# Performance work log

Hardware: AMD Instinct MI355X
Metric: run time of the kernel (lower is better)

The kernel has to match this reference:

```python
import jax, jax.numpy as jnp
import numpy as np

HEADS, DH, M_LAND, PINV_ITERS, LN_EPS = 8, 64, 256, 6, 1e-5


def layer_norm(x, g, b):
    mu = x.mean(-1, keepdims=True)
    var = ((x - mu) ** 2).mean(-1, keepdims=True)
    return (x - mu) * jax.lax.rsqrt(var + LN_EPS) * g + b


def moore_penrose_pinv(x, iters=PINV_ITERS):
    # x: (h, m, m). Iterative Newton-Schulz style pinv (lucidrains).
    abs_x = jnp.abs(x)
    col = abs_x.sum(-1)
    row = abs_x.sum(-2)
    z = jnp.swapaxes(x, -1, -2) / (jnp.max(col) * jnp.max(row))
    I = jnp.eye(x.shape[-1], dtype=x.dtype)
    for _ in range(iters):
        xz = x @ z
        z = 0.25 * z @ (13.0 * I - xz @ (15.0 * I - xz @ (7.0 * I - xz)))
    return z


def nystrom_attention(x, qkv_w, out_w, out_b, res_w):
    # x: (n, dim). No mask, eval mode (dropout off).
    n, dim = x.shape
    pad = (-n) % M_LAND
    xp = jnp.pad(x, ((pad, 0), (0, 0)))  # pad at sequence START, as in original
    n_p = n + pad
    l = n_p // M_LAND  # tokens per landmark
    qkv = xp @ qkv_w  # (n_p, 3*h*dh)
    q, k, v = jnp.split(qkv, 3, axis=-1)
    split = lambda t: t.reshape(n_p, HEADS, DH).transpose(1, 0, 2)  # (h, n_p, dh)
    q, k, v = split(q), split(k), split(v)
    q = q * (DH ** -0.5)
    q_l = q.reshape(HEADS, M_LAND, l, DH).mean(axis=2)  # (h, m, dh)
    k_l = k.reshape(HEADS, M_LAND, l, DH).mean(axis=2)
    sim1 = jnp.einsum('hid,hjd->hij', q, k_l)    # (h, n_p, m)
    sim2 = jnp.einsum('hid,hjd->hij', q_l, k_l)  # (h, m, m)
    sim3 = jnp.einsum('hid,hjd->hij', q_l, k)    # (h, m, n_p)
    a1 = jax.nn.softmax(sim1, axis=-1)
    a2 = jax.nn.softmax(sim2, axis=-1)
    a3 = jax.nn.softmax(sim3, axis=-1)
    a2_inv = moore_penrose_pinv(a2)
    out = a1 @ (a2_inv @ (a3 @ v))  # (h, n_p, dh)
    # residual depthwise conv over sequence dim, kernel 33, per head
    res = jax.lax.conv_general_dilated(
        v[None], res_w, (1, 1), ((16, 16), (0, 0)),
        feature_group_count=HEADS, dimension_numbers=('NCHW', 'OIHW', 'NCHW'))[0]
    out = out + res
    out = out.transpose(1, 0, 2).reshape(n_p, HEADS * DH)
    out = out @ out_w + out_b
    return out[-n:]  # drop the leading pad


def ppeg(x, w7, b7, w5, b5, w3, b3, H, W):
    cls_tok, feat = x[0], x[1:]
    C = feat.shape[1]
    img = feat.T.reshape(1, C, H, W)
    def dw(w, b, p):
        y = jax.lax.conv_general_dilated(
            img, w, (1, 1), ((p, p), (p, p)),
            feature_group_count=C, dimension_numbers=('NCHW', 'OIHW', 'NCHW'))
        return y + b.reshape(1, C, 1, 1)
    out = img + dw(w7, b7, 3) + dw(w5, b5, 2) + dw(w3, b3, 1)
    out = out[0].reshape(C, H * W).T
    return jnp.concatenate([cls_tok[None], out], axis=0)


def forward(h, fc1_w, fc1_b, cls_token, l1_ln_g, l1_ln_b, l1_qkv_w, l1_out_w, l1_out_b, l1_res_w,
            conv7_w, conv7_b, conv5_w, conv5_b, conv3_w, conv3_b,
            l2_ln_g, l2_ln_b, l2_qkv_w, l2_out_w, l2_out_b, l2_res_w,
            norm_g, norm_b, fc2_w, fc2_b):
    x = jax.nn.relu(h @ fc1_w + fc1_b)  # (N, 512)
    N = x.shape[0]
    Hs = Ws = int(np.ceil(np.sqrt(N)))  # N chosen perfect square -> add_length == 0
    x = jnp.concatenate([cls_token, x], axis=0)  # (N+1, 512)
    x = x + nystrom_attention(layer_norm(x, l1_ln_g, l1_ln_b), l1_qkv_w, l1_out_w, l1_out_b, l1_res_w)
    x = ppeg(x, conv7_w, conv7_b, conv5_w, conv5_b, conv3_w, conv3_b, Hs, Ws)
    x = x + nystrom_attention(layer_norm(x, l2_ln_g, l2_ln_b), l2_qkv_w, l2_out_w, l2_out_b, l2_res_w)
    x = layer_norm(x, norm_g, norm_b)[0]  # cls token readout
    return x @ fc2_w + fc2_b  # (n_classes,)


def setup_inputs() -> dict:
    key = jax.random.key(0)
    ks = jax.random.split(key, 16)
    nrm = lambda k, s, sc=0.02: jax.random.normal(k, s, jnp.float32) * sc
    D = 512
    return {
        'h': jax.random.normal(ks[0], (16384, 2048), jnp.float32),
        'fc1_w': nrm(ks[1], (2048, D)), 'fc1_b': jnp.zeros((D,), jnp.float32),
        'cls_token': nrm(ks[2], (1, D), 1.0),
        'l1_ln_g': jnp.ones((D,), jnp.float32), 'l1_ln_b': jnp.zeros((D,), jnp.float32),
        'l1_qkv_w': nrm(ks[3], (D, 3 * D)),
        'l1_out_w': nrm(ks[4], (D, D)), 'l1_out_b': jnp.zeros((D,), jnp.float32),
        'l1_res_w': nrm(ks[5], (HEADS, 1, 33, 1), 0.05),
        'conv7_w': nrm(ks[6], (D, 1, 7, 7), 0.05), 'conv7_b': jnp.zeros((D,), jnp.float32),
        'conv5_w': nrm(ks[7], (D, 1, 5, 5), 0.05), 'conv5_b': jnp.zeros((D,), jnp.float32),
        'conv3_w': nrm(ks[8], (D, 1, 3, 3), 0.05), 'conv3_b': jnp.zeros((D,), jnp.float32),
        'l2_ln_g': jnp.ones((D,), jnp.float32), 'l2_ln_b': jnp.zeros((D,), jnp.float32),
        'l2_qkv_w': nrm(ks[9], (D, 3 * D)),
        'l2_out_w': nrm(ks[10], (D, D)), 'l2_out_b': jnp.zeros((D,), jnp.float32),
        'l2_res_w': nrm(ks[11], (HEADS, 1, 33, 1), 0.05),
        'norm_g': jnp.ones((D,), jnp.float32), 'norm_b': jnp.zeros((D,), jnp.float32),
        'fc2_w': nrm(ks[12], (D, 2)), 'fc2_b': jnp.zeros((2,), jnp.float32),
    }


def reference(h, fc1_w, fc1_b, cls_token, l1_ln_g, l1_ln_b, l1_qkv_w, l1_out_w, l1_out_b, l1_res_w,
              conv7_w, conv7_b, conv5_w, conv5_b, conv3_w, conv3_b,
              l2_ln_g, l2_ln_b, l2_qkv_w, l2_out_w, l2_out_b, l2_res_w,
              norm_g, norm_b, fc2_w, fc2_b):
    return forward(h, fc1_w, fc1_b, cls_token, l1_ln_g, l1_ln_b, l1_qkv_w, l1_out_w, l1_out_b, l1_res_w,
                   conv7_w, conv7_b, conv5_w, conv5_b, conv3_w, conv3_b,
                   l2_ln_g, l2_ln_b, l2_qkv_w, l2_out_w, l2_out_b, l2_res_w,
                   norm_g, norm_b, fc2_w, fc2_b)
```

## Files before the change

kernel.cpp:

```cpp
#include <hip/hip_runtime.h>
#include <cstddef>

#define NROWS 16385
#define NPAD  16640
#define PADT  255
#define DIM   512
#define HEADS 8
#define DH    64
#define NL    256
#define LCH   65
#define LCHUNK 65
#define SLACK 24
#define LDST  40
#define AST   72

typedef short bf16x8 __attribute__((ext_vector_type(8)));
typedef float f32x4  __attribute__((ext_vector_type(4)));

__device__ __forceinline__ float wsum(float v){
#pragma unroll
  for (int o = 32; o; o >>= 1) v += __shfl_xor(v, o);
  return v;
}
__device__ __forceinline__ float wmax(float v){
#pragma unroll
  for (int o = 32; o; o >>= 1) v = fmaxf(v, __shfl_xor(v, o));
  return v;
}

__device__ __forceinline__ void split2(float x, unsigned short &h, unsigned short &l){
  unsigned ux = __float_as_uint(x);
  unsigned rh = (ux + 0x7FFFu + ((ux >> 16) & 1u)) >> 16;
  h = (unsigned short)rh;
  float fh = __uint_as_float(rh << 16);
  float r = x - fh;
  unsigned ur = __float_as_uint(r);
  unsigned rl = (ur + 0x7FFFu + ((ur >> 16) & 1u)) >> 16;
  l = (unsigned short)rl;
}
__device__ __forceinline__ float bf2f(unsigned short h){
  return __uint_as_float((unsigned)h << 16);
}

__global__ __launch_bounds__(256) void gemm64_sp_kernel(
    const unsigned short* __restrict__ Ah, const unsigned short* __restrict__ Al,
    const unsigned short* __restrict__ Bth, const unsigned short* __restrict__ Btl,
    const unsigned short* __restrict__ IB1h, const unsigned short* __restrict__ IB1l,
    const unsigned short* __restrict__ IB2h, const unsigned short* __restrict__ IB2l,
    float* __restrict__ Cf,
    unsigned short* __restrict__ Crh, unsigned short* __restrict__ Crl,
    unsigned short* __restrict__ Cth, unsigned short* __restrict__ Ctl,
    int M, int N, int K, long sA, long sB, long sC,
    float aAcc, float cDiag, float c1, float c2)
{
  size_t zo = (size_t)blockIdx.z;
  Ah  += zo*sA; Al  += zo*sA;
  Bth += zo*sB; Btl += zo*sB;
  if (IB1h){ IB1h += zo*sA; IB1l += zo*sA; }
  if (IB2h){ IB2h += zo*sA; IB2l += zo*sA; }
  if (Cf)  Cf  += zo*sC;
  if (Crh){ Crh += zo*sC; Crl += zo*sC; }
  if (Cth){ Cth += zo*sC; Ctl += zo*sC; }
  __shared__ unsigned short LAh[64*LDST], LAl[64*LDST], LBh[64*LDST], LBl[64*LDST];
  const int t = threadIdx.x;
  const int wid = t >> 6, lane = t & 63;
  const int wr = wid >> 1, wc = wid & 1;
  const int l15 = lane & 15, kb = lane >> 4;
  const int bm = blockIdx.y << 6, bn = blockIdx.x << 6;
  const int r4 = t >> 2, kc = (t & 3) << 3;
  f32x4 acc[2][2];
#pragma unroll
  for (int i=0;i<2;++i)
#pragma unroll
    for (int j=0;j<2;++j) acc[i][j] = (f32x4){0.f,0.f,0.f,0.f};

  for (int k0 = 0; k0 < K; k0 += 32){
    __syncthreads();
    {
      int lo = r4*LDST + kc;
      *(uint4*)&LAh[lo] = *(const uint4*)&Ah[(size_t)(bm+r4)*K + k0 + kc];
      *(uint4*)&LAl[lo] = *(const uint4*)&Al[(size_t)(bm+r4)*K + k0 + kc];
      *(uint4*)&LBh[lo] = *(const uint4*)&Bth[(size_t)(bn+r4)*K + k0 + kc];
      *(uint4*)&LBl[lo] = *(const uint4*)&Btl[(size_t)(bn+r4)*K + k0 + kc];
    }
    __syncthreads();
    bf16x8 ah[2], al[2], bh[2], bl[2];
#pragma unroll
    for (int r=0;r<2;++r){
      int off = (wr*32 + r*16 + l15)*LDST + kb*8;
      ah[r] = *(const bf16x8*)&LAh[off];
      al[r] = *(const bf16x8*)&LAl[off];
    }
#pragma unroll
    for (int c2v=0;c2v<2;++c2v){
      int off = (wc*32 + c2v*16 + l15)*LDST + kb*8;
      bh[c2v] = *(const bf16x8*)&LBh[off];
      bl[c2v] = *(const bf16x8*)&LBl[off];
    }
#pragma unroll
    for (int r=0;r<2;++r)
#pragma unroll
      for (int c2v=0;c2v<2;++c2v){
        acc[r][c2v] = __builtin_amdgcn_mfma_f32_16x16x32_bf16(ah[r], bh[c2v], acc[r][c2v], 0,0,0);
        acc[r][c2v] = __builtin_amdgcn_mfma_f32_16x16x32_bf16(ah[r], bl[c2v], acc[r][c2v], 0,0,0);
        acc[r][c2v] = __builtin_amdgcn_mfma_f32_16x16x32_bf16(al[r], bh[c2v], acc[r][c2v], 0,0,0);
      }
  }
#pragma unroll
  for (int r=0;r<2;++r){
#pragma unroll
    for (int c2v=0;c2v<2;++c2v){
      int col = bn + wc*32 + c2v*16 + l15;
      int rb  = bm + wr*32 + r*16 + kb*4;
      float v[4];
#pragma unroll
      for (int e=0;e<4;++e){
        float x = aAcc*acc[r][c2v][e];
        int row = rb + e;
        if (cDiag != 0.f && row == col) x += cDiag;
        if (IB1h){
          size_t io = (size_t)row*K + col;
          x += c1*(bf2f(IB1h[io]) + bf2f(IB1l[io]));
        }
        if (IB2h){
          size_t io = (size_t)row*K + col;
          x += c2*(bf2f(IB2h[io]) + bf2f(IB2l[io]));
        }
        v[e] = x;
      }
      if (Cf){
#pragma unroll
        for (int e=0;e<4;++e) Cf[(size_t)(rb+e)*N + col] = v[e];
      }
      if (Crh){
#pragma unroll
        for (int e=0;e<4;++e){
          unsigned short hh, ll;
          split2(v[e], hh, ll);
          Crh[(size_t)(rb+e)*N + col] = hh;
          Crl[(size_t)(rb+e)*N + col] = ll;
        }
      }
      if (Cth){
        unsigned short h4[4], l4[4];
#pragma unroll
        for (int e=0;e<4;++e) split2(v[e], h4[e], l4[e]);
        uint2 uh, ul;
        uh.x = (unsigned)h4[0] | ((unsigned)h4[1]<<16);
        uh.y = (unsigned)h4[2] | ((unsigned)h4[3]<<16);
        ul.x = (unsigned)l4[0] | ((unsigned)l4[1]<<16);
        ul.y = (unsigned)l4[2] | ((unsigned)l4[3]<<16);
        *(uint2*)&Cth[(size_t)col*M + rb] = uh;
        *(uint2*)&Ctl[(size_t)col*M + rb] = ul;
      }
    }
  }
}

__global__ __launch_bounds__(256) void gemm_sb_kernel(
    const unsigned short* __restrict__ Ah, const unsigned short* __restrict__ Al,
    const unsigned short* __restrict__ BTh, const unsigned short* __restrict__ BTl,
    const float* __restrict__ bias, float* __restrict__ C,
    int M, int N, int K, int accum)
{
  __shared__ unsigned short LAh[128*LDST], LAl[128*LDST], LBh[128*LDST], LBl[128*LDST];
  const int t = threadIdx.x;
  const int bm = blockIdx.y << 7, bn = blockIdx.x << 7;
  const int wid = t >> 6, lane = t & 63;
  const int wr = wid >> 1, wc = wid & 1;
  const int l15 = lane & 15, kb = lane >> 4;
  const int sr = t >> 1, sc0 = (t & 1) << 4;
  f32x4 acc[4][4];
#pragma unroll
  for (int i=0;i<4;++i)
#pragma unroll
    for (int j=0;j<4;++j) acc[i][j] = (f32x4){0.f,0.f,0.f,0.f};

  const uint4 zz = make_uint4(0,0,0,0);
  for (int k0 = 0; k0 < K; k0 += 32){
    __syncthreads();
    {
      bool av = (bm + sr) < M;
      size_t ga = (size_t)(bm + sr)*K + k0 + sc0;
      uint4 a0 = av ? *(const uint4*)(Ah + ga)     : zz;
      uint4 a1 = av ? *(const uint4*)(Ah + ga + 8) : zz;
      uint4 a2 = av ? *(const uint4*)(Al + ga)     : zz;
      uint4 a3 = av ? *(const uint4*)(Al + ga + 8) : zz;
      size_t gb = (size_t)(bn + sr)*K + k0 + sc0;
      uint4 b0 = *(const uint4*)(BTh + gb);
      uint4 b1 = *(const uint4*)(BTh + gb + 8);
      uint4 b2 = *(const uint4*)(BTl + gb);
      uint4 b3 = *(const uint4*)(BTl + gb + 8);
      int lo = sr*LDST + sc0;
      *(uint4*)&LAh[lo] = a0; *(uint4*)&LAh[lo+8] = a1;
      *(uint4*)&LAl[lo] = a2; *(uint4*)&LAl[lo+8] = a3;
      *(uint4*)&LBh[lo] = b0; *(uint4*)&LBh[lo+8] = b1;
      *(uint4*)&LBl[lo] = b2; *(uint4*)&LBl[lo+8] = b3;
    }
    __syncthreads();
    bf16x8 ah[4], al[4], bh[4], bl[4];
#pragma unroll
    for (int ai=0; ai<4; ++ai){
      int off = (wr*64 + ai*16 + l15)*LDST + kb*8;
      ah[ai] = *(const bf16x8*)&LAh[off];
      al[ai] = *(const bf16x8*)&LAl[off];
    }
#pragma unroll
    for (int bj=0; bj<4; ++bj){
      int off = (wc*64 + bj*16 + l15)*LDST + kb*8;
      bh[bj] = *(const bf16x8*)&LBh[off];
      bl[bj] = *(const bf16x8*)&LBl[off];
    }
#pragma unroll
    for (int ai=0; ai<4; ++ai)
#pragma unroll
      for (int bj=0; bj<4; ++bj){
        acc[ai][bj] = __builtin_amdgcn_mfma_f32_16x16x32_bf16(ah[ai], bh[bj], acc[ai][bj], 0,0,0);
        acc[ai][bj] = __builtin_amdgcn_mfma_f32_16x16x32_bf16(ah[ai], bl[bj], acc[ai][bj], 0,0,0);
        acc[ai][bj] = __builtin_amdgcn_mfma_f32_16x16x32_bf16(al[ai], bh[bj], acc[ai][bj], 0,0,0);
      }
  }
#pragma unroll
  for (int ai=0; ai<4; ++ai){
#pragma unroll
    for (int bj=0; bj<4; ++bj){
      int col = bn + wc*64 + bj*16 + l15;
      float bv = bias ? bias[col] : 0.f;
#pragma unroll
      for (int r=0; r<4; ++r){
        int row = bm + wr*64 + ai*16 + kb*4 + r;
        if (row < M){
          float v = acc[ai][bj][r] + bv;
          if (accum) v += C[(size_t)row*N + col];
          C[(size_t)row*N + col] = v;
        }
      }
    }
  }
}

__global__ __launch_bounds__(256) void gemm_sbf_kernel(
    const float* __restrict__ A,
    const unsigned short* __restrict__ BTh, const unsigned short* __restrict__ BTl,
    const float* __restrict__ bias, float* __restrict__ C,
    int M, int N, int K, int relu, int ksplit)
{
  const int kLen = K / ksplit;
  const int kOff = blockIdx.z * kLen;
  if (ksplit > 1) C += (size_t)blockIdx.z * M * N;
  __shared__ unsigned short LAh[128*LDST], LAl[128*LDST], LBh[128*LDST], LBl[128*LDST];
  const int t = threadIdx.x;
  const int bm = blockIdx.y << 7, bn = blockIdx.x << 7;
  const int wid = t >> 6, lane = t & 63;
  const int wr = wid >> 1, wc = wid & 1;
  const int l15 = lane & 15, kb = lane >> 4;
  const int sr = t >> 1, sc0 = (t & 1) << 4;
  f32x4 acc[4][4];
#pragma unroll
  for (int i=0;i<4;++i)
#pragma unroll
    for (int j=0;j<4;++j) acc[i][j] = (f32x4){0.f,0.f,0.f,0.f};

  for (int k0 = kOff; k0 < kOff + kLen; k0 += 32){
    __syncthreads();
    {
      const float* ap = A + (size_t)(bm + sr)*K + k0 + sc0;
      float va[16];
      *(float4*)&va[0]  = ((const float4*)ap)[0];
      *(float4*)&va[4]  = ((const float4*)ap)[1];
      *(float4*)&va[8]  = ((const float4*)ap)[2];
      *(float4*)&va[12] = ((const float4*)ap)[3];
      int lo = sr*LDST + sc0;
      unsigned* dh = (unsigned*)&LAh[lo];
      unsigned* dl = (unsigned*)&LAl[lo];
#pragma unroll
      for (int q=0;q<8;++q){
        unsigned short h0,l0,h1,l1;
        split2(va[2*q],   h0, l0);
        split2(va[2*q+1], h1, l1);
        dh[q] = (unsigned)h0 | ((unsigned)h1 << 16);
        dl[q] = (unsigned)l0 | ((unsigned)l1 << 16);
      }
      size_t gb = (size_t)(bn + sr)*K + k0 + sc0;
      uint4 b0 = *(const uint4*)(BTh + gb);
      uint4 b1 = *(const uint4*)(BTh + gb + 8);
      uint4 b2 = *(const uint4*)(BTl + gb);
      uint4 b3 = *(const uint4*)(BTl + gb + 8);
      *(uint4*)&LBh[lo] = b0; *(uint4*)&LBh[lo+8] = b1;
      *(uint4*)&LBl[lo] = b2; *(uint4*)&LBl[lo+8] = b3;
    }
    __syncthreads();
    bf16x8 ah[4], al[4], bh[4], bl[4];
#pragma unroll
    for (int ai=0; ai<4; ++ai){
      int off = (wr*64 + ai*16 + l15)*LDST + kb*8;
      ah[ai] = *(const bf16x8*)&LAh[off];
      al[ai] = *(const bf16x8*)&LAl[off];
    }
#pragma unroll
    for (int bj=0; bj<4; ++bj){
      int off = (wc*64 + bj*16 + l15)*LDST + kb*8;
      bh[bj] = *(const bf16x8*)&LBh[off];
      bl[bj] = *(const bf16x8*)&LBl[off];
    }
#pragma unroll
    for (int ai=0; ai<4; ++ai)
#pragma unroll
      for (int bj=0; bj<4; ++bj){
        acc[ai][bj] = __builtin_amdgcn_mfma_f32_16x16x32_bf16(ah[ai], bh[bj], acc[ai][bj], 0,0,0);
        acc[ai][bj] = __builtin_amdgcn_mfma_f32_16x16x32_bf16(ah[ai], bl[bj], acc[ai][bj], 0,0,0);
        acc[ai][bj] = __builtin_amdgcn_mfma_f32_16x16x32_bf16(al[ai], bh[bj], acc[ai][bj], 0,0,0);
      }
  }
#pragma unroll
  for (int ai=0; ai<4; ++ai){
#pragma unroll
    for (int bj=0; bj<4; ++bj){
      int col = bn + wc*64 + bj*16 + l15;
      float bv = (bias && ksplit==1) ? bias[col] : 0.f;
#pragma unroll
      for (int r=0; r<4; ++r){
        int row = bm + wr*64 + ai*16 + kb*4 + r;
        float v = acc[ai][bj][r] + bv;
        if (relu && ksplit==1) v = fmaxf(v, 0.f);
        C[(size_t)row*N + col] = v;
      }
    }
  }
}

__global__ void fc1fix_kernel(const float* __restrict__ CP, const float* __restrict__ bias,
                              float* __restrict__ X)
{
  size_t i = (size_t)blockIdx.x*256 + threadIdx.x;
  float4 a = ((const float4*)CP)[i];
  float4 b = ((const float4*)CP)[i + 2097152];
  float4 bb = ((const float4*)bias)[i & 127];
  float4 o;
  o.x = fmaxf(a.x + b.x + bb.x, 0.f);
  o.y = fmaxf(a.y + b.y + bb.y, 0.f);
  o.z = fmaxf(a.z + b.z + bb.z, 0.f);
  o.w = fmaxf(a.w + b.w + bb.w, 0.f);
  ((float4*)X)[i] = o;
}

__global__ void wt_split_T_kernel(const float* __restrict__ W,
                                  unsigned short* __restrict__ BTh,
                                  unsigned short* __restrict__ BTl, int K, int N)
{
  int idx = blockIdx.x*256 + threadIdx.x;
  if (idx >= N*K) return;
  int n = idx / K, k = idx - n*K;
  unsigned short h, l;
  split2(W[(size_t)k*N + n], h, l);
  BTh[idx] = h; BTl[idx] = l;
}

__global__ void att_split_kernel(const float* __restrict__ ATT,
                                 unsigned short* __restrict__ Ah,
                                 unsigned short* __restrict__ Al)
{
  size_t i4 = (size_t)blockIdx.x*256 + threadIdx.x;
  size_t e = i4*4;
  int row = (int)(e >> 9);
  float4 v = make_float4(0.f,0.f,0.f,0.f);
  if (row < NROWS) v = *(const float4*)(ATT + (size_t)PADT*DIM + e);
  unsigned short h0,l0,h1,l1,h2,l2,h3,l3;
  split2(v.x,h0,l0); split2(v.y,h1,l1); split2(v.z,h2,l2); split2(v.w,h3,l3);
  uint2 uh, ul;
  uh.x = (unsigned)h0 | ((unsigned)h1<<16); uh.y = (unsigned)h2 | ((unsigned)h3<<16);
  ul.x = (unsigned)l0 | ((unsigned)l1<<16); ul.y = (unsigned)l2 | ((unsigned)l3<<16);
  *(uint2*)(Ah + e) = uh;
  *(uint2*)(Al + e) = ul;
}

__global__ __launch_bounds__(256) void ln_pad_sb_kernel(
    const float* __restrict__ X, const float* __restrict__ g,
    const float* __restrict__ b, unsigned short* __restrict__ Yh,
    unsigned short* __restrict__ Yl)
{
  int p = blockIdx.x;
  int t = threadIdx.x;
  size_t base = (size_t)p*DIM;
  if (p < PADT){
    Yh[base+t] = 0; Yh[base+t+256] = 0;
    Yl[base+t] = 0; Yl[base+t+256] = 0;
    return;
  }
  const float* xr = X + (size_t)(p-PADT)*DIM;
  float x0 = xr[t], x1 = xr[t+256];
  float s = x0 + x1, sq = x0*x0 + x1*x1;
  s = wsum(s); sq = wsum(sq);
  __shared__ float rs[4], rq[4];
  if ((t&63)==0){ rs[t>>6]=s; rq[t>>6]=sq; }
  __syncthreads();
  float S = rs[0]+rs[1]+rs[2]+rs[3];
  float SQ = rq[0]+rq[1]+rq[2]+rq[3];
  float mu = S * (1.f/DIM);
  float var = SQ * (1.f/DIM) - mu*mu;
  float r = rsqrtf(var + 1e-5f);
  float y0 = (x0-mu)*r*g[t]     + b[t];
  float y1 = (x1-mu)*r*g[t+256] + b[t+256];
  unsigned short h, l;
  split2(y0, h, l); Yh[base+t] = h;     Yl[base+t] = l;
  split2(y1, h, l); Yh[base+t+256] = h; Yl[base+t+256] = l;
}

__global__ void landmarks_kernel(const float* __restrict__ QKV,
                                 float* __restrict__ QL, float* __restrict__ KL,
                                 unsigned short* __restrict__ KLh,
                                 unsigned short* __restrict__ KLl)
{
  int m = blockIdx.x, h = blockIdx.y, d = threadIdx.x;
  float sq = 0.f, sk = 0.f;
  const float* base = QKV + (size_t)(m*LCH)*1536 + (h<<6) + d;
  for (int j = 0; j < LCH; ++j){
    sq += base[0];
    sk += base[512];
    base += 1536;
  }
  size_t off = (((size_t)(h<<8)+m)<<6) + d;
  float klv = sk * (1.f/65.f);
  QL[off] = sq * (0.125f/65.f);
  KL[off] = klv;
  unsigned short hh, ll;
  split2(klv, hh, ll);
  KLh[off] = hh; KLl[off] = ll;
}

__global__ __launch_bounds__(256) void sim2_kernel(
    const float* __restrict__ QL, const float* __restrict__ KL, float* __restrict__ A2)
{
  int m = blockIdx.x, h = blockIdx.y, n = threadIdx.x;
  __shared__ float ql[64];
  __shared__ float red[4];
  if (n < 64) ql[n] = QL[(((h<<8)+m)<<6) + n];
  __syncthreads();
  const float* kl = KL + (size_t)(((h<<8)+n)<<6);
  float s = 0.f;
#pragma unroll
  for (int d=0; d<64; ++d) s += ql[d]*kl[d];
  float mx = wmax(s);
  if ((n&63)==0) red[n>>6] = mx;
  __syncthreads();
  mx = fmaxf(fmaxf(red[0],red[1]), fmaxf(red[2],red[3]));
  float e = __expf(s - mx);
  float sm = wsum(e);
  __syncthreads();
  if ((n&63)==0) red[n>>6] = sm;
  __syncthreads();
  sm = red[0]+red[1]+red[2]+red[3];
  A2[((size_t)((h<<8)+m)<<8) + n] = e/sm;
}

__global__ void crsum_kernel(const float* __restrict__ A2, float* __restrict__ CR)
{
  int b = blockIdx.x, t = threadIdx.x;
  float v;
  if (b < 2048){
    v = fabsf(A2[((size_t)b<<8) + t]);
  } else {
    int r = b - 2048;
    int h = r >> 8, n = r & 255;
    v = fabsf(A2[((size_t)h<<16) + (t<<8) + n]);
  }
  v = wsum(v);
  __shared__ float red[4];
  if ((t&63)==0) red[t>>6]=v;
  __syncthreads();
  if (t==0) CR[b] = red[0]+red[1]+red[2]+red[3];
}
__global__ void maxprod_kernel(const float* __restrict__ CR, float* __restrict__ SCAL)
{
  int t = threadIdx.x;
  float mc = -3e38f, mr = -3e38f;
  for (int i=t; i<2048; i+=256){ mc = fmaxf(mc, CR[i]); mr = fmaxf(mr, CR[2048+i]); }
  mc = wmax(mc); mr = wmax(mr);
  __shared__ float rc[4], rr[4];
  if ((t&63)==0){ rc[t>>6]=mc; rr[t>>6]=mr; }
  __syncthreads();
  if (t==0){
    float a = fmaxf(fmaxf(rc[0],rc[1]),fmaxf(rc[2],rc[3]));
    float b = fmaxf(fmaxf(rr[0],rr[1]),fmaxf(rr[2],rr[3]));
    SCAL[0] = 1.f/(a*b);
  }
}

__global__ void tsplit_kernel(const float* __restrict__ A2, const float* __restrict__ SCAL,
                              unsigned short* __restrict__ A2h, unsigned short* __restrict__ A2l,
                              unsigned short* __restrict__ Zrh, unsigned short* __restrict__ Zrl,
                              unsigned short* __restrict__ Zth, unsigned short* __restrict__ Ztl)
{
  int idx = blockIdx.x*256 + threadIdx.x;
  int h = idx >> 16, rem = idx & 65535, m = rem >> 8, n = rem & 255;
  float a = A2[idx];
  unsigned short hh, ll;
// ... 353 lines not shown
__global__ void zero_slack_kernel(float* __restrict__ QKV)
{
  int i = blockIdx.x*256 + threadIdx.x;
  QKV[(size_t)NPAD*1536 + i] = 0.f;
}

__global__ __launch_bounds__(256) void convres2_kernel(
    const float* __restrict__ QKV, const float* __restrict__ rw,
    float* __restrict__ ATT)
{
  const int t = threadIdx.x;
  const int c = blockIdx.y*256 + t;
  const int i0 = PADT + (blockIdx.x << 2);
  const int h = c >> 6;
  float w[33];
#pragma unroll
  for (int k=0;k<33;++k) w[k] = rw[h*33 + k];
  float acc[4] = {0.f,0.f,0.f,0.f};
  const float* vbase = QKV + (size_t)(i0-16)*1536 + 1024 + c;
#pragma unroll
  for (int rr=0; rr<36; ++rr){
    float v = vbase[(size_t)rr*1536];
#pragma unroll
    for (int k=0;k<4;++k){
      int tap = rr - k;
      if (tap >= 0 && tap <= 32) acc[k] += w[tap]*v;
    }
  }
#pragma unroll
  for (int k=0;k<4;++k){
    int i = i0 + k;
    if (i < NPAD) ATT[(size_t)i*DIM + c] += acc[k];
  }
}

__global__ void pad_kernel(const float* __restrict__ X, float* __restrict__ PIM)
{
  int r = blockIdx.x;
  int c = blockIdx.y*256 + threadIdx.x;
  int py = r / 134, px = r - py*134;
  float v = 0.f;
  if (py>=3 && py<131 && px>=3 && px<131)
    v = X[(size_t)(1 + (py-3)*128 + (px-3))*512 + c];
  PIM[(size_t)r*512 + c] = v;
}

__global__ void wtrans_kernel(const float* __restrict__ w7, const float* __restrict__ w5,
                              const float* __restrict__ w3, float* __restrict__ W7T,
                              float* __restrict__ W5T, float* __restrict__ W3T)
{
  int i = blockIdx.x;
  int c = blockIdx.y*256 + threadIdx.x;
  if (i < 49)      W7T[i*512+c]      = w7[c*49+i];
  else if (i < 74) W5T[(i-49)*512+c] = w5[c*25+(i-49)];
  else             W3T[(i-74)*512+c] = w3[c*9+(i-74)];
}

__global__ __launch_bounds__(256) void ppeg2_kernel(
    const float* __restrict__ PIM, const float* __restrict__ W7T,
    const float* __restrict__ W5T, const float* __restrict__ W3T,
    const float* __restrict__ b7, const float* __restrict__ b5,
    const float* __restrict__ b3, float* __restrict__ X2)
{
  const int t = threadIdx.x;
  const int c = blockIdx.z*256 + t;
  const int x = blockIdx.x;
  const int y0 = blockIdx.y << 2;
  float w7r[49], w5r[25], w3r[9];
#pragma unroll
  for (int i=0;i<49;++i) w7r[i] = W7T[i*512 + c];
#pragma unroll
  for (int i=0;i<25;++i) w5r[i] = W5T[i*512 + c];
#pragma unroll
  for (int i=0;i<9;++i)  w3r[i] = W3T[i*512 + c];
  const float bsum = b7[c] + b5[c] + b3[c];
  float acc[4] = {bsum, bsum, bsum, bsum};
  const float* base = PIM + ((size_t)(y0*134 + x))*512 + c;
#pragma unroll
  for (int rr=0; rr<10; ++rr){
#pragma unroll
    for (int cc=0; cc<7; ++cc){
      float v = base[(size_t)(rr*134 + cc)*512];
#pragma unroll
      for (int k=0;k<4;++k){
        const int dy = rr - k - 3, dx = cc - 3;
        if (dy >= -3 && dy <= 3){
          acc[k] += w7r[(dy+3)*7 + (dx+3)] * v;
          if (dy >= -2 && dy <= 2 && dx >= -2 && dx <= 2)
            acc[k] += w5r[(dy+2)*5 + (dx+2)] * v;
          if (dy >= -1 && dy <= 1 && dx >= -1 && dx <= 1)
            acc[k] += w3r[(dy+1)*3 + (dx+1)] * v;
          if (dy == 0 && dx == 0) acc[k] += v;
        }
      }
    }
  }
#pragma unroll
  for (int k=0;k<4;++k)
    X2[(size_t)(1 + (y0+k)*128 + x)*512 + c] = acc[k];
}

__global__ void copy_row_kernel(const float* __restrict__ src, float* __restrict__ dst)
{
  dst[threadIdx.x] = src[threadIdx.x];
}

__global__ void final_kernel(const float* __restrict__ X, const float* __restrict__ g,
                             const float* __restrict__ b, const float* __restrict__ fw,
                             const float* __restrict__ fb, float* __restrict__ out)
{
  int t = threadIdx.x;
  float x0 = X[t], x1 = X[t+256];
  float s = x0 + x1, sq = x0*x0 + x1*x1;
  s = wsum(s); sq = wsum(sq);
  __shared__ float rs[4], rq[4];
  if ((t&63)==0){ rs[t>>6]=s; rq[t>>6]=sq; }
  __syncthreads();
  float S = rs[0]+rs[1]+rs[2]+rs[3];
  float SQ = rq[0]+rq[1]+rq[2]+rq[3];
  float mu = S*(1.f/DIM);
  float var = SQ*(1.f/DIM) - mu*mu;
  float r = rsqrtf(var + 1e-5f);
  float n0 = (x0-mu)*r*g[t]     + b[t];
  float n1 = (x1-mu)*r*g[t+256] + b[t+256];
  float p0 = n0*fw[t*2]   + n1*fw[(t+256)*2];
  float p1 = n0*fw[t*2+1] + n1*fw[(t+256)*2+1];
  p0 = wsum(p0); p1 = wsum(p1);
  __shared__ float r0[4], r1[4];
  if ((t&63)==0){ r0[t>>6]=p0; r1[t>>6]=p1; }
  __syncthreads();
  if (t==0){
    out[0] = r0[0]+r0[1]+r0[2]+r0[3] + fb[0];
    out[1] = r1[0]+r1[1]+r1[2]+r1[3] + fb[1];
  }
}

struct Bufs {
  float *Y, *QKV, *QL, *KL, *A2, *CR, *SCAL, *PACC, *PML, *W7T, *W5T, *W3T;
  unsigned short *Yh, *Yl, *ATh, *ATl, *qBTh, *qBTl, *oBTh, *oBTl, *fBTh, *fBTl;
  unsigned short *A2h, *A2l, *XZrh, *XZrl, *XZth, *XZtl, *Wth, *Wtl, *W2th, *W2tl;
  unsigned short *Z0rh, *Z0rl, *Z0th, *Z0tl, *Z1rh, *Z1rl, *Z1th, *Z1tl;
  unsigned short *TMth, *TMtl, *KLh, *KLl, *BMth, *BMtl;
};

static void attention_layer(float* X, const float* ln_g, const float* ln_b,
                            const float* qkv_w, const float* out_w, const float* out_b,
                            const float* res_w, Bufs& bf, hipStream_t stream)
{
  const long SP = 65536;
  wt_split_T_kernel<<<(1536*512)/256, 256, 0, stream>>>(qkv_w, bf.qBTh, bf.qBTl, 512, 1536);
  wt_split_T_kernel<<<(512*512)/256, 256, 0, stream>>>(out_w, bf.oBTh, bf.oBTl, 512, 512);
  ln_pad_sb_kernel<<<NPAD, 256, 0, stream>>>(X, ln_g, ln_b, bf.Yh, bf.Yl);
  gemm_sb_kernel<<<dim3(12,130),256,0,stream>>>(bf.Yh, bf.Yl, bf.qBTh, bf.qBTl,
      nullptr, bf.QKV, NPAD, 1536, 512, 0);
  landmarks_kernel<<<dim3(NL,HEADS),64,0,stream>>>(bf.QKV, bf.QL, bf.KL, bf.KLh, bf.KLl);
  sim2_kernel<<<dim3(NL,HEADS),256,0,stream>>>(bf.QL, bf.KL, bf.A2);
  crsum_kernel<<<4096,256,0,stream>>>(bf.A2, bf.CR);
  maxprod_kernel<<<1,256,0,stream>>>(bf.CR, bf.SCAL);
  tsplit_kernel<<<2048,256,0,stream>>>(bf.A2, bf.SCAL, bf.A2h, bf.A2l,
      bf.Z0rh, bf.Z0rl, bf.Z0th, bf.Z0tl);
  unsigned short *Zarh=bf.Z0rh, *Zarl=bf.Z0rl, *Zath=bf.Z0th, *Zatl=bf.Z0tl;
  unsigned short *Zbrh=bf.Z1rh, *Zbrl=bf.Z1rl, *Zbth=bf.Z1th, *Zbtl=bf.Z1tl;
  for (int it = 0; it < 6; ++it){
    gemm64_sp_kernel<<<dim3(4,4,8),256,0,stream>>>(bf.A2h, bf.A2l, Zath, Zatl,
        nullptr,nullptr, nullptr,nullptr, nullptr,
        bf.XZrh, bf.XZrl, bf.XZth, bf.XZtl,
        256,256,256, SP,SP,SP, 1.f, 0.f, 0.f, 0.f);
    gemm64_sp_kernel<<<dim3(4,4,8),256,0,stream>>>(bf.XZrh, bf.XZrl, bf.XZth, bf.XZtl,
        nullptr,nullptr, nullptr,nullptr, nullptr,
        bf.Wth, bf.Wtl, bf.W2th, bf.W2tl,
        256,256,256, SP,SP,SP, 1.f, 0.f, 0.f, 0.f);
    gemm64_sp_kernel<<<dim3(4,4,8),256,0,stream>>>(bf.XZrh, bf.XZrl, bf.W2th, bf.W2tl,
        bf.XZrh, bf.XZrl, bf.Wth, bf.Wtl, nullptr,
        nullptr, nullptr, bf.XZth, bf.XZtl,
        256,256,256, SP,SP,SP, -1.f, 13.f, -15.f, 7.f);
    gemm64_sp_kernel<<<dim3(4,4,8),256,0,stream>>>(Zarh, Zarl, bf.XZth, bf.XZtl,
        nullptr,nullptr, nullptr,nullptr, nullptr,
        Zbrh, Zbrl, Zbth, Zbtl,
        256,256,256, SP,SP,SP, 0.25f, 0.f, 0.f, 0.f);
    unsigned short* tp;
    tp=Zarh; Zarh=Zbrh; Zbrh=tp;  tp=Zarl; Zarl=Zbrl; Zbrl=tp;
    tp=Zath; Zath=Zbth; Zbth=tp;  tp=Zatl; Zatl=Zbtl; Zbtl=tp;
  }
  lattn3_kernel<<<dim3(LCHUNK,4,HEADS),256,0,stream>>>(bf.QKV, bf.QL, bf.PACC, bf.PML);
  lattn_combine_kernel<<<2048,64,0,stream>>>(bf.PACC, bf.PML, bf.TMth, bf.TMtl);
  gemm64_sp_kernel<<<dim3(1,4,8),256,0,stream>>>(Zarh, Zarl, bf.TMth, bf.TMtl,
      nullptr,nullptr, nullptr,nullptr, nullptr,
      nullptr, nullptr, bf.BMth, bf.BMtl,
      256,64,256, SP, 16384L, 16384L, 1.f, 0.f, 0.f, 0.f);
  float* ATT = bf.Y;
  attn3_kernel<<<dim3(257,HEADS),256,0,stream>>>(bf.QKV, bf.KLh, bf.KLl,
      bf.BMth, bf.BMtl, ATT);
  convres2_kernel<<<dim3(4097,2),256,0,stream>>>(bf.QKV, res_w, ATT);
  att_split_kernel<<<8256,256,0,stream>>>(ATT, bf.ATh, bf.ATl);
  gemm_sb_kernel<<<dim3(4,129),256,0,stream>>>(bf.ATh, bf.ATl, bf.oBTh, bf.oBTl,
      out_b, X, NROWS, 512, 512, 1);
}

extern "C" void kernel_launch(void* const* d_in, const int* in_sizes, int n_in,
                              void* d_out, int out_size, void* d_ws, size_t ws_size,
                              hipStream_t stream)
{
  (void)in_sizes; (void)n_in; (void)out_size; (void)ws_size;
  const float* h       = (const float*)d_in[0];
  const float* fc1_w   = (const float*)d_in[1];
  const float* fc1_b   = (const float*)d_in[2];
  const float* cls     = (const float*)d_in[3];
  const float* l1_ln_g = (const float*)d_in[4];
  const float* l1_ln_b = (const float*)d_in[5];
  const float* l1_qkv_w= (const float*)d_in[6];
  const float* l1_out_w= (const float*)d_in[7];
  const float* l1_out_b= (const float*)d_in[8];
  const float* l1_res_w= (const float*)d_in[9];
  const float* conv7_w = (const float*)d_in[10];
  const float* conv7_b = (const float*)d_in[11];
  const float* conv5_w = (const float*)d_in[12];
  const float* conv5_b = (const float*)d_in[13];
  const float* conv3_w = (const float*)d_in[14];
  const float* conv3_b = (const float*)d_in[15];
  const float* l2_ln_g = (const float*)d_in[16];
  const float* l2_ln_b = (const float*)d_in[17];
  const float* l2_qkv_w= (const float*)d_in[18];
  const float* l2_out_w= (const float*)d_in[19];
  const float* l2_out_b= (const float*)d_in[20];
  const float* l2_res_w= (const float*)d_in[21];
  const float* norm_g  = (const float*)d_in[22];
  const float* norm_b  = (const float*)d_in[23];
  const float* fc2_w   = (const float*)d_in[24];
  const float* fc2_b   = (const float*)d_in[25];

  float* ws = (float*)d_ws;
  float* X   = ws;                 ws += (size_t)NROWS*DIM;
  float* X2  = ws;                 ws += (size_t)NROWS*DIM;
  Bufs bf;
  bf.Y    = ws;                    ws += (size_t)NPAD*DIM;
  bf.QKV  = ws;                    ws += (size_t)(NPAD+SLACK)*1536;
  bf.QL   = ws;                    ws += HEADS*NL*DH;
  bf.KL   = ws;                    ws += HEADS*NL*DH;
  bf.A2   = ws;                    ws += HEADS*NL*NL;
  bf.CR   = ws;                    ws += 4096;
  bf.SCAL = ws;                    ws += 8;
  bf.PACC = ws;                    ws += (size_t)LCHUNK*HEADS*NL*DH;
  bf.PML  = ws;                    ws += (size_t)LCHUNK*HEADS*NL*2;
  bf.W7T  = ws;                    ws += 49*512;
  bf.W5T  = ws;                    ws += 25*512;
  bf.W3T  = ws;                    ws += 9*512;
  unsigned short* us = (unsigned short*)ws;
  bf.Yh   = us;                    us += (size_t)NPAD*DIM;
  bf.Yl   = us;                    us += (size_t)NPAD*DIM;
  bf.ATh  = us;                    us += (size_t)16512*DIM;
  bf.ATl  = us;                    us += (size_t)16512*DIM;
  bf.qBTh = us;                    us += 1536*512;
  bf.qBTl = us;                    us += 1536*512;
  bf.oBTh = us;                    us += 512*512;
  bf.oBTl = us;                    us += 512*512;
  bf.fBTh = us;                    us += 512*2048;
  bf.fBTl = us;                    us += 512*2048;
  const size_t PL = (size_t)HEADS*NL*NL;
  bf.A2h  = us; us += PL;  bf.A2l  = us; us += PL;
  bf.XZrh = us; us += PL;  bf.XZrl = us; us += PL;
  bf.XZth = us; us += PL;  bf.XZtl = us; us += PL;
  bf.Wth  = us; us += PL;  bf.Wtl  = us; us += PL;
  bf.W2th = us; us += PL;  bf.W2tl = us; us += PL;
  bf.Z0rh = us; us += PL;  bf.Z0rl = us; us += PL;
  bf.Z0th = us; us += PL;  bf.Z0tl = us; us += PL;
  bf.Z1rh = us; us += PL;  bf.Z1rl = us; us += PL;
  bf.Z1th = us; us += PL;  bf.Z1tl = us; us += PL;
  bf.TMth = us; us += (size_t)HEADS*NL*DH;
  bf.TMtl = us; us += (size_t)HEADS*NL*DH;
  bf.KLh  = us; us += (size_t)HEADS*NL*DH;
  bf.KLl  = us; us += (size_t)HEADS*NL*DH;
  bf.BMth = us; us += (size_t)HEADS*NL*DH;
  bf.BMtl = us; us += (size_t)HEADS*NL*DH;
  float* PIM = bf.QKV;
  float* CP  = bf.Y;

  zero_slack_kernel<<<(SLACK*1536)/256, 256, 0, stream>>>(bf.QKV);
  wtrans_kernel<<<dim3(83,2),256,0,stream>>>(conv7_w, conv5_w, conv3_w,
                                             bf.W7T, bf.W5T, bf.W3T);

  wt_split_T_kernel<<<(512*2048)/256, 256, 0, stream>>>(fc1_w, bf.fBTh, bf.fBTl, 2048, 512);
  gemm_sbf_kernel<<<dim3(4,128,2),256,0,stream>>>(h, bf.fBTh, bf.fBTl, nullptr, CP,
      16384, 512, 2048, 0, 2);
  fc1fix_kernel<<<8192,256,0,stream>>>(CP, fc1_b, X + DIM);
  copy_row_kernel<<<1,512,0,stream>>>(cls, X);

  attention_layer(X, l1_ln_g, l1_ln_b, l1_qkv_w, l1_out_w, l1_out_b, l1_res_w, bf, stream);

  pad_kernel<<<dim3(17956,2),256,0,stream>>>(X, PIM);
  ppeg2_kernel<<<dim3(128,32,2),256,0,stream>>>(PIM, bf.W7T, bf.W5T, bf.W3T,
                                                conv7_b, conv5_b, conv3_b, X2);
  copy_row_kernel<<<1,512,0,stream>>>(X, X2);

  attention_layer(X2, l2_ln_g, l2_ln_b, l2_qkv_w, l2_out_w, l2_out_b, l2_res_w, bf, stream);

  final_kernel<<<1,256,0,stream>>>(X2, norm_g, norm_b, fc2_w, fc2_b, (float*)d_out);
}
```

Measured before the change: 2.006 ms.

## Pre-split fc1 input to bf16 pairs and restructure pinv Newton-Schulz GEMM chain

The fc1 projection stops converting fp32 input to hi/lo bf16 inside a split-K GEMM. A separate hsplit pass now writes the split input, and the shared gemm_sb kernel runs without split-K, applying bias and ReLU in its epilogue, which removes the partial-sum buffer and the fixup kernel. Separately, the pinv iteration's GEMM chain is reorganised so each GEMM folds a scaled identity and a residual add into its epilogue (7I - xz, 15I - xz·W, and so on), which changes the operand flow. The fc1 change adds an extra full read/write pass over the 16384x2048 input and loses split-K parallelism (512 blocks instead of 1024).

Measured after the change: 1.991 ms. No clear change (-0.7%).

```diff
diff --git a/kernel.cpp b/kernel.cpp
--- a/kernel.cpp
+++ b/kernel.cpp
@@ -161,7 +161,7 @@
     const unsigned short* __restrict__ Ah, const unsigned short* __restrict__ Al,
     const unsigned short* __restrict__ BTh, const unsigned short* __restrict__ BTl,
     const float* __restrict__ bias, float* __restrict__ C,
-    int M, int N, int K, int accum)
+    int M, int N, int K, int accum, int relu)
 {
   __shared__ unsigned short LAh[128*LDST], LAl[128*LDST], LBh[128*LDST], LBl[128*LDST];
   const int t = threadIdx.x;
@@ -232,6 +232,7 @@
         if (row < M){
           float v = acc[ai][bj][r] + bv;
           if (accum) v += C[(size_t)row*N + col];
+          if (relu) v = fmaxf(v, 0.f);
           C[(size_t)row*N + col] = v;
         }
       }
@@ -239,109 +240,19 @@
   }
 }
 
-__global__ __launch_bounds__(256) void gemm_sbf_kernel(
-    const float* __restrict__ A,
-    const unsigned short* __restrict__ BTh, const unsigned short* __restrict__ BTl,
-    const float* __restrict__ bias, float* __restrict__ C,
-    int M, int N, int K, int relu, int ksplit)
-{
-  const int kLen = K / ksplit;
-  const int kOff = blockIdx.z * kLen;
-  if (ksplit > 1) C += (size_t)blockIdx.z * M * N;
-  __shared__ unsigned short LAh[128*LDST], LAl[128*LDST], LBh[128*LDST], LBl[128*LDST];
-  const int t = threadIdx.x;
-  const int bm = blockIdx.y << 7, bn = blockIdx.x << 7;
-  const int wid = t >> 6, lane = t & 63;
-  const int wr = wid >> 1, wc = wid & 1;
-  const int l15 = lane & 15, kb = lane >> 4;
-  const int sr = t >> 1, sc0 = (t & 1) << 4;
-  f32x4 acc[4][4];
-#pragma unroll
-  for (int i=0;i<4;++i)
-#pragma unroll
-    for (int j=0;j<4;++j) acc[i][j] = (f32x4){0.f,0.f,0.f,0.f};
-
-  for (int k0 = kOff; k0 < kOff + kLen; k0 += 32){
-    __syncthreads();
-    {
-      const float* ap = A + (size_t)(bm + sr)*K + k0 + sc0;
-      float va[16];
-      *(float4*)&va[0]  = ((const float4*)ap)[0];
-      *(float4*)&va[4]  = ((const float4*)ap)[1];
-      *(float4*)&va[8]  = ((const float4*)ap)[2];
-      *(float4*)&va[12] = ((const float4*)ap)[3];
-      int lo = sr*LDST + sc0;
-      unsigned* dh = (unsigned*)&LAh[lo];
-      unsigned* dl = (unsigned*)&LAl[lo];
-#pragma unroll
-      for (int q=0;q<8;++q){
-        unsigned short h0,l0,h1,l1;
-        split2(va[2*q],   h0, l0);
-        split2(va[2*q+1], h1, l1);
-        dh[q] = (unsigned)h0 | ((unsigned)h1 << 16);
-        dl[q] = (unsigned)l0 | ((unsigned)l1 << 16);
-      }
-      size_t gb = (size_t)(bn + sr)*K + k0 + sc0;
-      uint4 b0 = *(const uint4*)(BTh + gb);
-      uint4 b1 = *(const uint4*)(BTh + gb + 8);
-      uint4 b2 = *(const uint4*)(BTl + gb);
-      uint4 b3 = *(const uint4*)(BTl + gb + 8);
-      *(uint4*)&LBh[lo] = b0; *(uint4*)&LBh[lo+8] = b1;
-      *(uint4*)&LBl[lo] = b2; *(uint4*)&LBl[lo+8] = b3;
-    }
-    __syncthreads();
-    bf16x8 ah[4], al[4], bh[4], bl[4];
-#pragma unroll
-    for (int ai=0; ai<4; ++ai){
-      int off = (wr*64 + ai*16 + l15)*LDST + kb*8;
-      ah[ai] = *(const bf16x8*)&LAh[off];
-      al[ai] = *(const bf16x8*)&LAl[off];
-    }
-#pragma unroll
-    for (int bj=0; bj<4; ++bj){
-      int off = (wc*64 + bj*16 + l15)*LDST + kb*8;
-      bh[bj] = *(const bf16x8*)&LBh[off];
-      bl[bj] = *(const bf16x8*)&LBl[off];
-    }
-#pragma unroll
-    for (int ai=0; ai<4; ++ai)
-#pragma unroll
-      for (int bj=0; bj<4; ++bj){
-        acc[ai][bj] = __builtin_amdgcn_mfma_f32_16x16x32_bf16(ah[ai], bh[bj], acc[ai][bj], 0,0,0);
-        acc[ai][bj] = __builtin_amdgcn_mfma_f32_16x16x32_bf16(ah[ai], bl[bj], acc[ai][bj], 0,0,0);
-        acc[ai][bj] = __builtin_amdgcn_mfma_f32_16x16x32_bf16(al[ai], bh[bj], acc[ai][bj], 0,0,0);
-      }
-  }
-#pragma unroll
-  for (int ai=0; ai<4; ++ai){
-#pragma unroll
-    for (int bj=0; bj<4; ++bj){
-      int col = bn + wc*64 + bj*16 + l15;
-      float bv = (bias && ksplit==1) ? bias[col] : 0.f;
-#pragma unroll
-      for (int r=0; r<4; ++r){
-        int row = bm + wr*64 + ai*16 + kb*4 + r;
-        float v = acc[ai][bj][r] + bv;
-        if (relu && ksplit==1) v = fmaxf(v, 0.f);
-        C[(size_t)row*N + col] = v;
-      }
-    }
-  }
-}
-
-__global__ void fc1fix_kernel(const float* __restrict__ CP, const float* __restrict__ bias,
-                              float* __restrict__ X)
+__global__ void hsplit_kernel(const float* __restrict__ H,
+                              unsigned short* __restrict__ Ah,
+                              unsigned short* __restrict__ Al)
 {
   size_t i = (size_t)blockIdx.x*256 + threadIdx.x;
-  float4 a = ((const float4*)CP)[i];
-  float4 b = ((const float4*)CP)[i + 2097152];
-  float4 bb = ((const float4*)bias)[i & 127];
-  float4 o;
-  o.x = fmaxf(a.x + b.x + bb.x, 0.f);
-  o.y = fmaxf(a.y + b.y + bb.y, 0.f);
-  o.z = fmaxf(a.z + b.z + bb.z, 0.f);
-  o.w = fmaxf(a.w + b.w + bb.w, 0.f);
-  ((float4*)X)[i] = o;
+  float4 v = ((const float4*)H)[i];
+  unsigned short h0,l0,h1,l1,h2,l2,h3,l3;
+  split2(v.x,h0,l0); split2(v.y,h1,l1); split2(v.z,h2,l2); split2(v.w,h3,l3);
+  uint2 uh, ul;
+  uh.x = (unsigned)h0 | ((unsigned)h1<<16); uh.y = (unsigned)h2 | ((unsigned)h3<<16);
+  ul.x = (unsigned)l0 | ((unsigned)l1<<16); ul.y = (unsigned)l2 | ((unsigned)l3<<16);
+  *(uint2*)(Ah + i*4) = uh;
+  *(uint2*)(Al + i*4) = ul;
 }
 
 __global__ void wt_split_T_kernel(const float* __restrict__ W,
@@ -1001,7 +912,7 @@
   wt_split_T_kernel<<<(512*512)/256, 256, 0, stream>>>(out_w, bf.oBTh, bf.oBTl, 512, 512);
   ln_pad_sb_kernel<<<NPAD, 256, 0, stream>>>(X, ln_g, ln_b, bf.Yh, bf.Yl);
   gemm_sb_kernel<<<dim3(12,130),256,0,stream>>>(bf.Yh, bf.Yl, bf.qBTh, bf.qBTl,
-      nullptr, bf.QKV, NPAD, 1536, 512, 0);
+      nullptr, bf.QKV, NPAD, 1536, 512, 0, 0);
   landmarks_kernel<<<dim3(NL,HEADS),64,0,stream>>>(bf.QKV, bf.QL, bf.KL, bf.KLh, bf.KLl);
   sim2_kernel<<<dim3(NL,HEADS),256,0,stream>>>(bf.QL, bf.KL, bf.A2);
   crsum_kernel<<<4096,256,0,stream>>>(bf.A2, bf.CR);
@@ -1016,17 +927,17 @@
         bf.XZrh, bf.XZrl, bf.XZth, bf.XZtl,
         256,256,256, SP,SP,SP, 1.f, 0.f, 0.f, 0.f);
     gemm64_sp_kernel<<<dim3(4,4,8),256,0,stream>>>(bf.XZrh, bf.XZrl, bf.XZth, bf.XZtl,
-        nullptr,nullptr, nullptr,nullptr, nullptr,
-        bf.Wth, bf.Wtl, bf.W2th, bf.W2tl,
-        256,256,256, SP,SP,SP, 1.f, 0.f, 0.f, 0.f);
-    gemm64_sp_kernel<<<dim3(4,4,8),256,0,stream>>>(bf.XZrh, bf.XZrl, bf.W2th, bf.W2tl,
-        bf.XZrh, bf.XZrl, bf.Wth, bf.Wtl, nullptr,
-        nullptr, nullptr, bf.XZth, bf.XZtl,
-        256,256,256, SP,SP,SP, -1.f, 13.f, -15.f, 7.f);
-    gemm64_sp_kernel<<<dim3(4,4,8),256,0,stream>>>(Zarh, Zarl, bf.XZth, bf.XZtl,
-        nullptr,nullptr, nullptr,nullptr, nullptr,
+        bf.XZrh, bf.XZrl, nullptr,nullptr, nullptr,
+        nullptr, nullptr, bf.Wth, bf.Wtl,
+        256,256,256, SP,SP,SP, -1.f, 0.f, 7.f, 0.f);
+    gemm64_sp_kernel<<<dim3(4,4,8),256,0,stream>>>(bf.XZrh, bf.XZrl, bf.Wth, bf.Wtl,
+        bf.XZrh, bf.XZrl, nullptr,nullptr, nullptr,
+        nullptr, nullptr, bf.W2th, bf.W2tl,
+        256,256,256, SP,SP,SP, -1.f, 0.f, 15.f, 0.f);
+    gemm64_sp_kernel<<<dim3(4,4,8),256,0,stream>>>(Zarh, Zarl, bf.W2th, bf.W2tl,
+        Zarh, Zarl, nullptr,nullptr, nullptr,
         Zbrh, Zbrl, Zbth, Zbtl,
-        256,256,256, SP,SP,SP, 0.25f, 0.f, 0.f, 0.f);
+        256,256,256, SP,SP,SP, -0.25f, 0.f, 3.25f, 0.f);
     unsigned short* tp;
     tp=Zarh; Zarh=Zbrh; Zbrh=tp;  tp=Zarl; Zarl=Zbrl; Zbrl=tp;
     tp=Zath; Zath=Zbth; Zbth=tp;  tp=Zatl; Zatl=Zbtl; Zbtl=tp;
@@ -1043,7 +954,7 @@
   convres2_kernel<<<dim3(4097,2),256,0,stream>>>(bf.QKV, res_w, ATT);
   att_split_kernel<<<8256,256,0,stream>>>(ATT, bf.ATh, bf.ATl);
   gemm_sb_kernel<<<dim3(4,129),256,0,stream>>>(bf.ATh, bf.ATl, bf.oBTh, bf.oBTl,
-      out_b, X, NROWS, 512, 512, 1);
+      out_b, X, NROWS, 512, 512, 1, 0);
 }
 
 extern "C" void kernel_launch(void* const* d_in, const int* in_sizes, int n_in,
@@ -1122,16 +1033,17 @@
   bf.BMth = us; us += (size_t)HEADS*NL*DH;
   bf.BMtl = us; us += (size_t)HEADS*NL*DH;
   float* PIM = bf.QKV;
-  float* CP  = bf.Y;
+  unsigned short* hAh = (unsigned short*)bf.Y;
+  unsigned short* hAl = hAh + (size_t)16384*2048;
 
   zero_slack_kernel<<<(SLACK*1536)/256, 256, 0, stream>>>(bf.QKV);
   wtrans_kernel<<<dim3(83,2),256,0,stream>>>(conv7_w, conv5_w, conv3_w,
                                              bf.W7T, bf.W5T, bf.W3T);
 
   wt_split_T_kernel<<<(512*2048)/256, 256, 0, stream>>>(fc1_w, bf.fBTh, bf.fBTl, 2048, 512);
-  gemm_sbf_kernel<<<dim3(4,128,2),256,0,stream>>>(h, bf.fBTh, bf.fBTl, nullptr, CP,
-      16384, 512, 2048, 0, 2);
-  fc1fix_kernel<<<8192,256,0,stream>>>(CP, fc1_b, X + DIM);
+  hsplit_kernel<<<32768,256,0,stream>>>(h, hAh, hAl);
+  gemm_sb_kernel<<<dim3(4,128),256,0,stream>>>(hAh, hAl, bf.fBTh, bf.fBTl,
+      fc1_b, X + DIM, 16384, 512, 2048, 0, 1);
   copy_row_kernel<<<1,512,0,stream>>>(cls, X);
 
   attention_layer(X, l1_ln_g, l1_ln_b, l1_qkv_w, l1_out_w, l1_out_b, l1_res_w, bf, stream);
```
